# Optimization experiments

Measured on AMD Instinct MI355X. Metric: run time of the kernel, lower is better.

Reference implementation:

```python
import jax, jax.numpy as jnp
import numpy as np

N_NODES = 100000
N_EDGES = 1600000
D = 64


def _sage_conv(x, src, dst, W_l, W_r, b):
    # PyG SAGEConv (aggr='mean'): out_i = W_l @ mean_{j in N(i)} x_j + W_r @ x_i + b
    n = x.shape[0]
    msgs = x[src]  # [E, D] gather of source-node features
    agg = jax.ops.segment_sum(msgs, dst, num_segments=n)  # [N, D]
    cnt = jax.ops.segment_sum(jnp.ones((src.shape[0],), x.dtype), dst, num_segments=n)
    mean = agg / jnp.maximum(cnt, 1.0)[:, None]
    return mean @ W_l.T + x @ W_r.T + b


def setup_inputs() -> dict:
    key = jax.random.key(0)
    ks = jax.random.split(key, 8)
    s = 1.0 / np.sqrt(D)
    x = jax.random.normal(ks[0], (N_NODES, D), dtype=jnp.float32)
    edge_index = jax.random.randint(ks[1], (2, N_EDGES), 0, N_NODES, dtype=jnp.int64)
    return {
        "x": x,
        "edge_index": edge_index,
        "W1_l": jax.random.normal(ks[2], (D, D), dtype=jnp.float32) * s,
        "W1_r": jax.random.normal(ks[3], (D, D), dtype=jnp.float32) * s,
        "b1": jnp.zeros((D,), dtype=jnp.float32),
        "W2_l": jax.random.normal(ks[4], (D, D), dtype=jnp.float32) * s,
        "W2_r": jax.random.normal(ks[5], (D, D), dtype=jnp.float32) * s,
        "b2": jnp.zeros((D,), dtype=jnp.float32),
    }


def reference(x, edge_index, W1_l, W1_r, b1, W2_l, W2_r, b2):
    src, dst = edge_index[0], edge_index[1]
    h = _sage_conv(x, src, dst, W1_l, W1_r, b1)
    h = jax.nn.relu(h)
    out = _sage_conv(h, src, dst, W2_l, W2_r, b2)
    return out
```

## Files before the change

### kernel.cpp

```cpp
#include <hip/hip_runtime.h>

#define D 64
#define BSHIFT 9
#define BNODES (1 << BSHIFT)
#define NBK_MAX 512

typedef __attribute__((ext_vector_type(8))) short bf16x8;
typedef __attribute__((ext_vector_type(4))) float f32x4;

__device__ __forceinline__ unsigned int f2bf_rne(float f) {
    unsigned int b = __float_as_uint(f);
    return (b + 0x7fffu + ((b >> 16) & 1u)) >> 16;
}
__device__ __forceinline__ unsigned int pack_bf(float lo, float hi) {
    return f2bf_rne(lo) | (f2bf_rne(hi) << 16);
}
__device__ __forceinline__ float bflo(unsigned int u) { return __uint_as_float(u << 16); }
__device__ __forceinline__ float bfhi(unsigned int u) { return __uint_as_float(u & 0xffff0000u); }

__global__ void zeroi_kernel(int* __restrict__ p, int n) {
    int i = blockIdx.x * blockDim.x + threadIdx.x;
    if (i < n) p[i] = 0;
}

__global__ void cast_kernel(const float4* __restrict__ xin, uint2* __restrict__ xb, int n4) {
    int i = blockIdx.x * blockDim.x + threadIdx.x;
    int stride = gridDim.x * blockDim.x;
    for (; i < n4; i += stride) {
        float4 v = xin[i];
        uint2 o;
        o.x = pack_bf(v.x, v.y);
        o.y = pack_bf(v.z, v.w);
        xb[i] = o;
    }
}

__global__ __launch_bounds__(256) void hist2_kernel(const int* __restrict__ dst,
                                                    int* __restrict__ cnt2,
                                                    int E, int NBK, int CE) {
    __shared__ int lh[NBK_MAX];
    for (int k = threadIdx.x; k < NBK; k += 256) lh[k] = 0;
    __syncthreads();
    int b = blockIdx.x, g = b & 7;
    int beg = b * CE, end = min(beg + CE, E);
    for (int e = beg + threadIdx.x; e < end; e += 256)
        atomicAdd(&lh[dst[e] >> BSHIFT], 1);
    __syncthreads();
    for (int k = threadIdx.x; k < NBK; k += 256)
        if (lh[k]) atomicAdd(&cnt2[(k << 3) | g], lh[k]);
}

__global__ __launch_bounds__(256) void scan2k_kernel(const int* __restrict__ cnt2,
                                                     int* __restrict__ cur2,
                                                     int* __restrict__ bstart, int NBK) {
    __shared__ int s[256];
    int n = NBK << 3;
    int per = (n + 255) / 256;
    int tid = threadIdx.x;
    int base = tid * per;
    int loc[32];
    int sum = 0;
    for (int j = 0; j < per; ++j) {
        int idx = base + j;
        int v = (idx < n) ? cnt2[idx] : 0;
        loc[j] = sum;
        sum += v;
    }
    s[tid] = sum;
    __syncthreads();
    for (int off = 1; off < 256; off <<= 1) {
        int t = (tid >= off) ? s[tid - off] : 0;
        __syncthreads();
        s[tid] += t;
        __syncthreads();
    }
    int ebase = s[tid] - sum;
    for (int j = 0; j < per; ++j) {
        int idx = base + j;
        if (idx < n) {
            int e = ebase + loc[j];
            cur2[idx] = e;
            if ((idx & 7) == 0) bstart[idx >> 3] = e;
        }
    }
    if (tid == 0) bstart[NBK] = s[255];
}

__global__ __launch_bounds__(256) void binscatter_kernel(
    const int* __restrict__ src, const int* __restrict__ dst,
    int* __restrict__ cur2, unsigned int* __restrict__ pairs,
    int E, int NBK, int CE) {
    __shared__ int lh[NBK_MAX];
    __shared__ int lbase[NBK_MAX];
    for (int k = threadIdx.x; k < NBK; k += 256) lh[k] = 0;
    __syncthreads();
    int b = blockIdx.x, g = b & 7;
    int beg = b * CE, end = min(beg + CE, E);
    for (int e = beg + threadIdx.x; e < end; e += 256)
        atomicAdd(&lh[dst[e] >> BSHIFT], 1);
    __syncthreads();
    for (int k = threadIdx.x; k < NBK; k += 256) {
        int c = lh[k];
        if (c) lbase[k] = atomicAdd(&cur2[(k << 3) | g], c);
        lh[k] = 0;
    }
    __syncthreads();
    for (int e = beg + threadIdx.x; e < end; e += 256) {
        int d = dst[e];
        int k = d >> BSHIFT;
        int r = atomicAdd(&lh[k], 1);
        pairs[lbase[k] + r] = (unsigned int)src[e] | ((unsigned int)(d & (BNODES - 1)) << 17);
    }
}

__global__ __launch_bounds__(256) void csr_build_kernel(
    const unsigned int* __restrict__ pairs, const int* __restrict__ bstart,
    int* __restrict__ rowptr, int* __restrict__ csr, int N, int NBK) {
    __shared__ int lcnt[BNODES];
    __shared__ int lofs[BNODES];
    __shared__ int s[256];
    int k = blockIdx.x;
    int tid = threadIdx.x;
    int node0 = k << BSHIFT;
    int nnodes = min(BNODES, N - node0);
    int rbeg = bstart[k], rend = bstart[k + 1];

    for (int j = tid; j < BNODES; j += 256) lcnt[j] = 0;
    __syncthreads();
    for (int i = rbeg + tid; i < rend; i += 256)
        atomicAdd(&lcnt[pairs[i] >> 17], 1);
    __syncthreads();
    int v0 = lcnt[2 * tid], v1 = lcnt[2 * tid + 1];
    int ps = v0 + v1;
    s[tid] = ps;
    __syncthreads();
    for (int off = 1; off < 256; off <<= 1) {
        int t = (tid >= off) ? s[tid - off] : 0;
        __syncthreads();
        s[tid] += t;
        __syncthreads();
    }
    int ebase = s[tid] - ps;
    lofs[2 * tid] = ebase;
    lofs[2 * tid + 1] = ebase + v0;
    __syncthreads();
    for (int j = tid; j < nnodes; j += 256) {
        int p = rbeg + lofs[j];
        rowptr[node0 + j] = p;
        lcnt[j] = p;
    }
    if (k == NBK - 1 && tid == 0) rowptr[N] = rend;
    __syncthreads();
    for (int i = rbeg + tid; i < rend; i += 256) {
        unsigned int rec = pairs[i];
        int j = rec >> 17;
        int pos = atomicAdd(&lcnt[j], 1);
        csr[pos] = (int)(rec & 0x1FFFFu);
    }
}

__global__ __launch_bounds__(256) void agg_bf_kernel(
    const unsigned int* __restrict__ xb, const int* __restrict__ rowptr,
    const int* __restrict__ csr, unsigned int* __restrict__ meanb, int N) {
    int lane = threadIdx.x & 63;
    int q  = lane >> 3;
    int fl = lane & 7;
    int wid = blockIdx.x * (blockDim.x >> 6) + (threadIdx.x >> 6);
    int nwaves = gridDim.x * (blockDim.x >> 6);
    int noct = (N + 7) >> 3;

    for (int p = wid; p < noct; p += nwaves) {
        int node = p * 8 + q;
        bool valid = node < N;
        int beg = 0, end = 0;
        if (valid) { beg = rowptr[node]; end = rowptr[node + 1]; }
        float s0 = 0.f, s1 = 0.f, s2 = 0.f, s3 = 0.f;
        float s4 = 0.f, s5 = 0.f, s6 = 0.f, s7 = 0.f;
        int j = beg;
        for (; j + 4 <= end; j += 4) {
            int i0 = csr[j], i1 = csr[j + 1], i2 = csr[j + 2], i3 = csr[j + 3];
            uint4 u0 = *(const uint4*)(xb + i0 * 32 + fl * 4);
            uint4 u1 = *(const uint4*)(xb + i1 * 32 + fl * 4);
            uint4 u2 = *(const uint4*)(xb + i2 * 32 + fl * 4);
            uint4 u3 = *(const uint4*)(xb + i3 * 32 + fl * 4);
            s0 += bflo(u0.x) + bflo(u1.x) + bflo(u2.x) + bflo(u3.x);
            s1 += bfhi(u0.x) + bfhi(u1.x) + bfhi(u2.x) + bfhi(u3.x);
            s2 += bflo(u0.y) + bflo(u1.y) + bflo(u2.y) + bflo(u3.y);
            s3 += bfhi(u0.y) + bfhi(u1.y) + bfhi(u2.y) + bfhi(u3.y);
            s4 += bflo(u0.z) + bflo(u1.z) + bflo(u2.z) + bflo(u3.z);
            s5 += bfhi(u0.z) + bfhi(u1.z) + bfhi(u2.z) + bfhi(u3.z);
            s6 += bflo(u0.w) + bflo(u1.w) + bflo(u2.w) + bflo(u3.w);
            s7 += bfhi(u0.w) + bfhi(u1.w) + bfhi(u2.w) + bfhi(u3.w);
        }
        for (; j < end; ++j) {
            uint4 u = *(const uint4*)(xb + csr[j] * 32 + fl * 4);
            s0 += bflo(u.x); s1 += bfhi(u.x);
            s2 += bflo(u.y); s3 += bfhi(u.y);
            s4 += bflo(u.z); s5 += bfhi(u.z);
            s6 += bflo(u.w); s7 += bfhi(u.w);
        }
        if (valid) {
            float inv = 1.0f / fmaxf((float)(end - beg), 1.0f);
            uint4 o;
            o.x = pack_bf(s0 * inv, s1 * inv);
            o.y = pack_bf(s2 * inv, s3 * inv);
            o.z = pack_bf(s4 * inv, s5 * inv);
            o.w = pack_bf(s6 * inv, s7 * inv);
            *(uint4*)(meanb + node * 32 + fl * 4) = o;
        }
    }
}

__global__ __launch_bounds__(256) void lin_mfma_kernel(
    const unsigned int* __restrict__ meanb, const unsigned int* __restrict__ xin,
    const float* __restrict__ Wl, const float* __restrict__ Wr,
    const float* __restrict__ bias,
    float* __restrict__ outf, unsigned int* __restrict__ outb, int N, int relu) {
    int tid = threadIdx.x;
    int ft   = tid >> 6;
    int lane = tid & 63;
    int lm   = lane & 15;
    int quad = lane >> 4;

    int f_a = ft * 16 + lm;
    bf16x8 wh[4], wlo[4];
#pragma unroll
    for (int s = 0; s < 4; ++s) {
        int k8 = s * 32 + quad * 8;
        const float* Wsrc = (k8 < 64) ? Wl : Wr;
        const float* p = Wsrc + f_a * 64 + (k8 & 63);
        float4 w0 = *(const float4*)p;
        float4 w1 = *(const float4*)(p + 4);
        float w[8] = {w0.x, w0.y, w0.z, w0.w, w1.x, w1.y, w1.z, w1.w};
        bf16x8 h, l;
#pragma unroll
        for (int j = 0; j < 8; ++j) {
            unsigned int hb = f2bf_rne(w[j]);
            float hf = __uint_as_float(hb << 16);
            unsigned int lb = f2bf_rne(w[j] - hf);
            h[j] = (short)hb;
            l[j] = (short)lb;
        }
        wh[s] = h;
        wlo[s] = l;
    }

    int node0 = blockIdx.x * 64;
    f32x4 acc[4];
#pragma unroll
    for (int nt = 0; nt < 4; ++nt) acc[nt] = (f32x4){0.f, 0.f, 0.f, 0.f};

#pragma unroll
    for (int nt = 0; nt < 4; ++nt) {
        int node = node0 + nt * 16 + lm;
        bool v = node < N;
        const unsigned int* mrow = meanb + (long long)node * 32;
        const unsigned int* xrow = xin   + (long long)node * 32;
#pragma unroll
        for (int s = 0; s < 4; ++s) {
            uint4 u = make_uint4(0u, 0u, 0u, 0u);
            if (v) {
                const unsigned int* srcrow = (s < 2) ? mrow : xrow;
                u = *(const uint4*)(srcrow + (s & 1) * 16 + quad * 4);
            }
            union { uint4 u4; bf16x8 v8; } cv;
            cv.u4 = u;
            acc[nt] = __builtin_amdgcn_mfma_f32_16x16x32_bf16(wh[s],  cv.v8, acc[nt], 0, 0, 0);
            acc[nt] = __builtin_amdgcn_mfma_f32_16x16x32_bf16(wlo[s], cv.v8, acc[nt], 0, 0, 0);
        }
    }

    int fb = ft * 16 + quad * 4;
    float4 bv = *(const float4*)(bias + fb);
#pragma unroll
    for (int nt = 0; nt < 4; ++nt) {
        int node = node0 + nt * 16 + lm;
        if (node >= N) continue;
        float r0 = acc[nt][0] + bv.x;
        float r1 = acc[nt][1] + bv.y;
        float r2 = acc[nt][2] + bv.z;
        float r3 = acc[nt][3] + bv.w;
        if (relu) {
            r0 = fmaxf(r0, 0.f); r1 = fmaxf(r1, 0.f);
            r2 = fmaxf(r2, 0.f); r3 = fmaxf(r3, 0.f);
        }
        if (outf) *(float4*)(outf + (long long)node * D + fb) = make_float4(r0, r1, r2, r3);
        if (outb) *(uint2*)(outb + (long long)node * 32 + (fb >> 1)) =
                      make_uint2(pack_bf(r0, r1), pack_bf(r2, r3));
    }
}

extern "C" void kernel_launch(void* const* d_in, const int* in_sizes, int n_in,
                              void* d_out, int out_size, void* d_ws, size_t ws_size,
                              hipStream_t stream) {
    const float* x   = (const float*)d_in[0];
    const int* ei    = (const int*)d_in[1];
    const float* W1l = (const float*)d_in[2];
    const float* W1r = (const float*)d_in[3];
    const float* b1  = (const float*)d_in[4];
    const float* W2l = (const float*)d_in[5];
    const float* W2r = (const float*)d_in[6];
    const float* b2  = (const float*)d_in[7];

    const int E = in_sizes[1] / 2;
    const int N = in_sizes[0] / D;
    const int* src  = ei;
    const int* dstp = ei + E;
    const int NBK = (N + BNODES - 1) >> BSHIFT;
    const int G1 = 512;
    const int CE = (E + G1 - 1) / G1;

    char* ws = (char*)d_ws;
    size_t off = 0;
    auto alloc = [&](size_t bytes) { void* p = ws + off; off = (off + bytes + 255) & ~(size_t)255; return p; };
    int* cnt2           = (int*)alloc((size_t)(NBK * 8) * 4);
    int* cur2           = (int*)alloc((size_t)(NBK * 8) * 4);
    int* bstart         = (int*)alloc((size_t)(NBK + 1) * 4);
    int* rowptr         = (int*)alloc((size_t)(N + 1) * 4);
    unsigned int* pairs = (unsigned int*)alloc((size_t)E * 4);
    int* csr            = (int*)alloc((size_t)E * 4);
    unsigned int* xb    = (unsigned int*)alloc((size_t)N * 32 * 4);
    unsigned int* meanb = (unsigned int*)alloc((size_t)N * 32 * 4);
    unsigned int* hb    = (unsigned int*)alloc((size_t)N * 32 * 4);

    float* out = (float*)d_out;

    cast_kernel<<<2048, 256, 0, stream>>>((const float4*)x, (uint2*)xb, N * 16);

    zeroi_kernel<<<(NBK * 8 + 255) / 256, 256, 0, stream>>>(cnt2, NBK * 8);
    hist2_kernel<<<G1, 256, 0, stream>>>(dstp, cnt2, E, NBK, CE);
    scan2k_kernel<<<1, 256, 0, stream>>>(cnt2, cur2, bstart, NBK);
    binscatter_kernel<<<G1, 256, 0, stream>>>(src, dstp, cur2, pairs, E, NBK, CE);
    csr_build_kernel<<<NBK, 256, 0, stream>>>(pairs, bstart, rowptr, csr, N, NBK);

    const int linGrid = (N + 63) / 64;

    agg_bf_kernel<<<4096, 256, 0, stream>>>(xb, rowptr, csr, meanb, N);
    lin_mfma_kernel<<<linGrid, 256, 0, stream>>>(meanb, xb, W1l, W1r, b1, nullptr, hb, N, 1);

    agg_bf_kernel<<<4096, 256, 0, stream>>>(hb, rowptr, csr, meanb, N);
    lin_mfma_kernel<<<linGrid, 256, 0, stream>>>(meanb, hb, W2l, W2r, b2, out, nullptr, N, 0);
}
```

Baseline: 267.8 us.

## Fuse neighbor aggregation with MFMA linear layer through shared memory

Merges the mean-aggregation kernel and the MFMA linear kernel into one per-layer kernel. Each block aggregates 64 nodes into an XOR-swizzled LDS tile, then feeds that tile straight into the MFMAs, which removes the meanb global write and reread and one launch per layer. It also folds the counter zeroing into the cast kernel to drop another launch. The cost is that aggregation now runs on a fixed grid of one block per 64 nodes instead of a persistent grid-stride loop, and the weight split and MFMA phase now wait behind a block-wide barrier.

```diff
diff --git a/kernel.cpp b/kernel.cpp
--- a/kernel.cpp
+++ b/kernel.cpp
@@ -18,15 +18,12 @@
 __device__ __forceinline__ float bflo(unsigned int u) { return __uint_as_float(u << 16); }
 __device__ __forceinline__ float bfhi(unsigned int u) { return __uint_as_float(u & 0xffff0000u); }
 
-__global__ void zeroi_kernel(int* __restrict__ p, int n) {
-    int i = blockIdx.x * blockDim.x + threadIdx.x;
-    if (i < n) p[i] = 0;
-}
-
-__global__ void cast_kernel(const float4* __restrict__ xin, uint2* __restrict__ xb, int n4) {
-    int i = blockIdx.x * blockDim.x + threadIdx.x;
+__global__ void cast_kernel(const float4* __restrict__ xin, uint2* __restrict__ xb, int n4,
+                            int* __restrict__ cnt2, int nz) {
+    int gid = blockIdx.x * blockDim.x + threadIdx.x;
+    if (gid < nz) cnt2[gid] = 0;
     int stride = gridDim.x * blockDim.x;
-    for (; i < n4; i += stride) {
+    for (int i = gid; i < n4; i += stride) {
         float4 v = xin[i];
         uint2 o;
         o.x = pack_bf(v.x, v.y);
@@ -99,6 +96,7 @@
     for (int e = beg + threadIdx.x; e < end; e += 256)
         atomicAdd(&lh[dst[e] >> BSHIFT], 1);
     __syncthreads();
+    for (int k = threadIdx.x; k < 256; k += 256) {}
     for (int k = threadIdx.x; k < NBK; k += 256) {
         int c = lh[k];
         if (c) lbase[k] = atomicAdd(&cur2[(k << 3) | g], c);
@@ -159,18 +157,24 @@
     }
 }
 
-__global__ __launch_bounds__(256) void agg_bf_kernel(
-    const unsigned int* __restrict__ xb, const int* __restrict__ rowptr,
-    const int* __restrict__ csr, unsigned int* __restrict__ meanb, int N) {
-    int lane = threadIdx.x & 63;
+__global__ __launch_bounds__(256) void fused_layer_kernel(
+    const unsigned int* __restrict__ xin, const int* __restrict__ rowptr,
+    const int* __restrict__ csr,
+    const float* __restrict__ Wl, const float* __restrict__ Wr,
+    const float* __restrict__ bias,
+    float* __restrict__ outf, unsigned int* __restrict__ outb, int N, int relu) {
+    __shared__ uint4 smean[64][8];
+
+    int tid = threadIdx.x;
+    int wave = tid >> 6;
+    int lane = tid & 63;
+    int node0 = blockIdx.x * 64;
+
     int q  = lane >> 3;
     int fl = lane & 7;
-    int wid = blockIdx.x * (blockDim.x >> 6) + (threadIdx.x >> 6);
-    int nwaves = gridDim.x * (blockDim.x >> 6);
-    int noct = (N + 7) >> 3;
-
-    for (int p = wid; p < noct; p += nwaves) {
-        int node = p * 8 + q;
+    for (int o = 0; o < 2; ++o) {
+        int nl = (wave << 4) + (o << 3) + q;
+        int node = node0 + nl;
         bool valid = node < N;
         int beg = 0, end = 0;
         if (valid) { beg = rowptr[node]; end = rowptr[node + 1]; }
@@ -179,10 +183,10 @@
         int j = beg;
         for (; j + 4 <= end; j += 4) {
             int i0 = csr[j], i1 = csr[j + 1], i2 = csr[j + 2], i3 = csr[j + 3];
-            uint4 u0 = *(const uint4*)(xb + i0 * 32 + fl * 4);
-            uint4 u1 = *(const uint4*)(xb + i1 * 32 + fl * 4);
-            uint4 u2 = *(const uint4*)(xb + i2 * 32 + fl * 4);
-            uint4 u3 = *(const uint4*)(xb + i3 * 32 + fl * 4);
+            uint4 u0 = *(const uint4*)(xin + i0 * 32 + fl * 4);
+            uint4 u1 = *(const uint4*)(xin + i1 * 32 + fl * 4);
+            uint4 u2 = *(const uint4*)(xin + i2 * 32 + fl * 4);
+            uint4 u3 = *(const uint4*)(xin + i3 * 32 + fl * 4);
             s0 += bflo(u0.x) + bflo(u1.x) + bflo(u2.x) + bflo(u3.x);
             s1 += bfhi(u0.x) + bfhi(u1.x) + bfhi(u2.x) + bfhi(u3.x);
             s2 += bflo(u0.y) + bflo(u1.y) + bflo(u2.y) + bflo(u3.y);
@@ -193,36 +197,24 @@
             s7 += bfhi(u0.w) + bfhi(u1.w) + bfhi(u2.w) + bfhi(u3.w);
         }
         for (; j < end; ++j) {
-            uint4 u = *(const uint4*)(xb + csr[j] * 32 + fl * 4);
+            uint4 u = *(const uint4*)(xin + csr[j] * 32 + fl * 4);
             s0 += bflo(u.x); s1 += bfhi(u.x);
             s2 += bflo(u.y); s3 += bfhi(u.y);
             s4 += bflo(u.z); s5 += bfhi(u.z);
             s6 += bflo(u.w); s7 += bfhi(u.w);
         }
-        if (valid) {
-            float inv = 1.0f / fmaxf((float)(end - beg), 1.0f);
-            uint4 o;
-            o.x = pack_bf(s0 * inv, s1 * inv);
-            o.y = pack_bf(s2 * inv, s3 * inv);
-            o.z = pack_bf(s4 * inv, s5 * inv);
-            o.w = pack_bf(s6 * inv, s7 * inv);
-            *(uint4*)(meanb + node * 32 + fl * 4) = o;
-        }
-    }
-}
-
-__global__ __launch_bounds__(256) void lin_mfma_kernel(
-    const unsigned int* __restrict__ meanb, const unsigned int* __restrict__ xin,
-    const float* __restrict__ Wl, const float* __restrict__ Wr,
-    const float* __restrict__ bias,
-    float* __restrict__ outf, unsigned int* __restrict__ outb, int N, int relu) {
-    int tid = threadIdx.x;
-    int ft   = tid >> 6;
-    int lane = tid & 63;
+        float inv = valid ? 1.0f / fmaxf((float)(end - beg), 1.0f) : 0.f;
+        uint4 ov;
+        ov.x = pack_bf(s0 * inv, s1 * inv);
+        ov.y = pack_bf(s2 * inv, s3 * inv);
+        ov.z = pack_bf(s4 * inv, s5 * inv);
+        ov.w = pack_bf(s6 * inv, s7 * inv);
+        smean[nl][fl ^ (nl & 7)] = ov;
+    }
+
     int lm   = lane & 15;
     int quad = lane >> 4;
-
-    int f_a = ft * 16 + lm;
+    int f_a  = (wave << 4) + lm;
     bf16x8 wh[4], wlo[4];
 #pragma unroll
     for (int s = 0; s < 4; ++s) {
@@ -234,35 +226,40 @@
         float w[8] = {w0.x, w0.y, w0.z, w0.w, w1.x, w1.y, w1.z, w1.w};
         bf16x8 h, l;
 #pragma unroll
-        for (int j = 0; j < 8; ++j) {
-            unsigned int hb = f2bf_rne(w[j]);
+        for (int jj = 0; jj < 8; ++jj) {
+            unsigned int hb = f2bf_rne(w[jj]);
             float hf = __uint_as_float(hb << 16);
-            unsigned int lb = f2bf_rne(w[j] - hf);
-            h[j] = (short)hb;
-            l[j] = (short)lb;
+            unsigned int lb = f2bf_rne(w[jj] - hf);
+            h[jj] = (short)hb;
+            l[jj] = (short)lb;
         }
         wh[s] = h;
         wlo[s] = l;
     }
 
-    int node0 = blockIdx.x * 64;
+    __syncthreads();
+
     f32x4 acc[4];
 #pragma unroll
     for (int nt = 0; nt < 4; ++nt) acc[nt] = (f32x4){0.f, 0.f, 0.f, 0.f};
 
 #pragma unroll
     for (int nt = 0; nt < 4; ++nt) {
-        int node = node0 + nt * 16 + lm;
+        int nl = nt * 16 + lm;
+        int node = node0 + nl;
         bool v = node < N;
-        const unsigned int* mrow = meanb + (long long)node * 32;
-        const unsigned int* xrow = xin   + (long long)node * 32;
-#pragma unroll
-        for (int s = 0; s < 4; ++s) {
+        const unsigned int* xrow = xin + (long long)node * 32;
+#pragma unroll
+        for (int s = 0; s < 2; ++s) {
+            union { uint4 u4; bf16x8 v8; } cv;
+            cv.u4 = smean[nl][(s * 4 + quad) ^ (lm & 7)];
+            acc[nt] = __builtin_amdgcn_mfma_f32_16x16x32_bf16(wh[s],  cv.v8, acc[nt], 0, 0, 0);
+            acc[nt] = __builtin_amdgcn_mfma_f32_16x16x32_bf16(wlo[s], cv.v8, acc[nt], 0, 0, 0);
+        }
+#pragma unroll
+        for (int s = 2; s < 4; ++s) {
             uint4 u = make_uint4(0u, 0u, 0u, 0u);
-            if (v) {
-                const unsigned int* srcrow = (s < 2) ? mrow : xrow;
-                u = *(const uint4*)(srcrow + (s & 1) * 16 + quad * 4);
-            }
+            if (v) u = *(const uint4*)(xrow + ((s & 1) << 4) + (quad << 2));
             union { uint4 u4; bf16x8 v8; } cv;
             cv.u4 = u;
             acc[nt] = __builtin_amdgcn_mfma_f32_16x16x32_bf16(wh[s],  cv.v8, acc[nt], 0, 0, 0);
@@ -270,7 +267,7 @@
         }
     }
 
-    int fb = ft * 16 + quad * 4;
+    int fb = (wave << 4) + quad * 4;
     float4 bv = *(const float4*)(bias + fb);
 #pragma unroll
     for (int nt = 0; nt < 4; ++nt) {
@@ -320,14 +317,12 @@
     unsigned int* pairs = (unsigned int*)alloc((size_t)E * 4);
     int* csr            = (int*)alloc((size_t)E * 4);
     unsigned int* xb    = (unsigned int*)alloc((size_t)N * 32 * 4);
-    unsigned int* meanb = (unsigned int*)alloc((size_t)N * 32 * 4);
     unsigned int* hb    = (unsigned int*)alloc((size_t)N * 32 * 4);
 
     float* out = (float*)d_out;
 
-    cast_kernel<<<2048, 256, 0, stream>>>((const float4*)x, (uint2*)xb, N * 16);
-
-    zeroi_kernel<<<(NBK * 8 + 255) / 256, 256, 0, stream>>>(cnt2, NBK * 8);
+    cast_kernel<<<2048, 256, 0, stream>>>((const float4*)x, (uint2*)xb, N * 16, cnt2, NBK * 8);
+
     hist2_kernel<<<G1, 256, 0, stream>>>(dstp, cnt2, E, NBK, CE);
     scan2k_kernel<<<1, 256, 0, stream>>>(cnt2, cur2, bstart, NBK);
     binscatter_kernel<<<G1, 256, 0, stream>>>(src, dstp, cur2, pairs, E, NBK, CE);
@@ -335,9 +330,8 @@
 
     const int linGrid = (N + 63) / 64;
 
-    agg_bf_kernel<<<4096, 256, 0, stream>>>(xb, rowptr, csr, meanb, N);
-    lin_mfma_kernel<<<linGrid, 256, 0, stream>>>(meanb, xb, W1l, W1r, b1, nullptr, hb, N, 1);
-
-    agg_bf_kernel<<<4096, 256, 0, stream>>>(hb, rowptr, csr, meanb, N);
-    lin_mfma_kernel<<<linGrid, 256, 0, stream>>>(meanb, hb, W2l, W2r, b2, out, nullptr, N, 0);
-}
+    fused_layer_kernel<<<linGrid, 256, 0, stream>>>(xb, rowptr, csr, W1l, W1r, b1,
+                                                    nullptr, hb, N, 1);
+    fused_layer_kernel<<<linGrid, 256, 0, stream>>>(hb, rowptr, csr, W2l, W2r, b2,
+                                                    out, nullptr, N, 0);
+}
```

Result: faster. 252.7 us (-5.6%).
